# Optimization experiments

Measured on AMD Instinct MI355X. Metric: run time of the kernel, lower is better.

Reference implementation:

```python
import jax, jax.numpy as jnp
import numpy as np

B, Q, CACHE, CROSS = 16, 16, 1024, 1024
D, H, DK, DFF = 1024, 16, 64, 4096
EPS = 1e-5


def _ln(x, g, b):
    mu = jnp.mean(x, axis=-1, keepdims=True)
    var = jnp.mean(jnp.square(x - mu), axis=-1, keepdims=True)
    return (x - mu) * jax.lax.rsqrt(var + EPS) * g + b


def _heads(t):  # [B, L, D] -> [B, H, L, DK]
    return t.reshape(t.shape[0], t.shape[1], H, DK).transpose(0, 2, 1, 3)


def _attn(q, k, v, mask):  # q:[B,H,Q,DK] k,v:[B,H,L,DK] mask:[B,Q,L] bool
    scores = jnp.einsum('bhqd,bhkd->bhqk', q, k) / np.sqrt(DK).astype(np.float32)
    scores = jnp.where(mask[:, None, :, :], scores, jnp.finfo(scores.dtype).min)
    p = jax.nn.softmax(scores, axis=-1)
    o = jnp.einsum('bhqk,bhkd->bhqd', p, v)
    return o.transpose(0, 2, 1, 3).reshape(q.shape[0], q.shape[2], D)


def setup_inputs() -> dict:
    key = jax.random.key(0)
    ks = jax.random.split(key, 24)
    s = 0.02
    inp = {
        'x': jax.random.normal(ks[0], (B, Q, D), jnp.float32),
        'self_k_cache': jax.random.normal(ks[1], (B, CACHE, D), jnp.float32),
        'self_v_cache': jax.random.normal(ks[2], (B, CACHE, D), jnp.float32),
        'cross_k': jax.random.normal(ks[3], (B, CROSS, D), jnp.float32),
        'cross_v': jax.random.normal(ks[4], (B, CROSS, D), jnp.float32),
        'self_attn_mask': jnp.ones((B, Q, CACHE), jnp.bool_),
        'cross_attn_mask': jnp.ones((B, Q, CROSS), jnp.bool_),
        'ln1_g': jnp.ones((D,), jnp.float32), 'ln1_b': jnp.zeros((D,), jnp.float32),
        'ln2_g': jnp.ones((D,), jnp.float32), 'ln2_b': jnp.zeros((D,), jnp.float32),
        'ln3_g': jnp.ones((D,), jnp.float32), 'ln3_b': jnp.zeros((D,), jnp.float32),
        'wq_s': jax.random.normal(ks[5], (D, D), jnp.float32) * s, 'bq_s': jnp.zeros((D,), jnp.float32),
        'wk_s': jax.random.normal(ks[6], (D, D), jnp.float32) * s, 'bk_s': jnp.zeros((D,), jnp.float32),
        'wv_s': jax.random.normal(ks[7], (D, D), jnp.float32) * s, 'bv_s': jnp.zeros((D,), jnp.float32),
        'wo_s': jax.random.normal(ks[8], (D, D), jnp.float32) * s, 'bo_s': jnp.zeros((D,), jnp.float32),
        'wq_c': jax.random.normal(ks[9], (D, D), jnp.float32) * s, 'bq_c': jnp.zeros((D,), jnp.float32),
        'wo_c': jax.random.normal(ks[10], (D, D), jnp.float32) * s, 'bo_c': jnp.zeros((D,), jnp.float32),
        'w1': jax.random.normal(ks[11], (D, DFF), jnp.float32) * s, 'b1': jnp.zeros((DFF,), jnp.float32),
        'w2': jax.random.normal(ks[12], (DFF, D), jnp.float32) * s, 'b2': jnp.zeros((D,), jnp.float32),
    }
    return inp


def reference(x, self_k_cache, self_v_cache, cross_k, cross_v,
              self_attn_mask, cross_attn_mask,
              ln1_g, ln1_b, ln2_g, ln2_b, ln3_g, ln3_b,
              wq_s, bq_s, wk_s, bk_s, wv_s, bv_s, wo_s, bo_s,
              wq_c, bq_c, wo_c, bo_c, w1, b1, w2, b2):
    # --- self-attention with KV-cache append ---
    xn = _ln(x, ln1_g, ln1_b)
    q = xn @ wq_s + bq_s
    k_new = xn @ wk_s + bk_s
    v_new = xn @ wv_s + bv_s
    k_cache = self_k_cache.at[:, CACHE - Q:, :].set(k_new)
    v_cache = self_v_cache.at[:, CACHE - Q:, :].set(v_new)
    sa = _attn(_heads(q), _heads(k_cache), _heads(v_cache), self_attn_mask)
    x = x + (sa @ wo_s + bo_s)
    # --- cross-attention (k, v pre-projected) ---
    xn = _ln(x, ln2_g, ln2_b)
    qc = xn @ wq_c + bq_c
    ca = _attn(_heads(qc), _heads(cross_k), _heads(cross_v), cross_attn_mask)
    x = x + (ca @ wo_c + bo_c)
    # --- MLP ---
    xn = _ln(x, ln3_g, ln3_b)
    x = x + (jax.nn.gelu(xn @ w1 + b1) @ w2 + b2)
    return (x, k_cache, v_cache)
```

## Files before the change

kernel.cpp:

```cpp
#include <hip/hip_runtime.h>
#include <math.h>

#define D 1024
#define QLEN 16
#define DKH 64
#define ASPLIT 4
#define LC 256

typedef unsigned int uint;
typedef unsigned short ushort;
typedef __attribute__((ext_vector_type(8))) short bf16x8;
typedef __attribute__((ext_vector_type(4))) float f32x4;

struct GemmPtrs {
  const void* W[3];
  const float* bias[3];
  const float* res[3];
  float* C[3];
};

struct WcvtDesc { const float* src; ushort* dst; int K; int N; };
struct WcvtArgs { WcvtDesc d[8]; };

__device__ __forceinline__ ushort f2bf(float f) {
  uint u = __float_as_uint(f);
  u += 0x7fffu + ((u >> 16) & 1u);
  return (ushort)(u >> 16);
}

__device__ __forceinline__ float gelu_tanh(float x) {
  float t = 0.7978845608028654f * (x + 0.044715f * x * x * x);
  float e = __expf(2.0f * t);
  float th = 1.0f - 2.0f / (e + 1.0f);
  return 0.5f * x * (1.0f + th);
}

__global__ __launch_bounds__(256)
void wcvt_k(WcvtArgs a) {
  WcvtDesc de = a.d[blockIdx.y];
  int ntn = de.N >> 6;
  int ntiles = (de.K >> 6) * ntn;
  int tile = blockIdx.x;
  if (tile >= ntiles) return;
  int kt = tile / ntn, nt = tile - kt * ntn;
  __shared__ ushort Ls[64][72];
  int t = threadIdx.x;
  int colf4 = t & 15, rbase = t >> 4;
  #pragma unroll
  for (int u = 0; u < 4; ++u) {
    int kl = u * 16 + rbase;
    float4 w4 = *(const float4*)(de.src + (size_t)(kt*64 + kl) * de.N + nt*64 + colf4*4);
    Ls[colf4*4 + 0][kl] = f2bf(w4.x);
    Ls[colf4*4 + 1][kl] = f2bf(w4.y);
    Ls[colf4*4 + 2][kl] = f2bf(w4.z);
    Ls[colf4*4 + 3][kl] = f2bf(w4.w);
  }
  __syncthreads();
  int nl = t >> 2, c = t & 3;
  uint4 v0 = *(const uint4*)(&Ls[nl][c*16]);
  uint4 v1 = *(const uint4*)(&Ls[nl][c*16 + 8]);
  ushort* dst = de.dst + (size_t)(nt*64 + nl) * de.K + kt*64 + c*16;
  *(uint4*)(dst)     = v0;
  *(uint4*)(dst + 8) = v1;
}

__global__ __launch_bounds__(256)
void ln_k(const float* __restrict__ X, const float* __restrict__ g,
          const float* __restrict__ be, uint* __restrict__ Yb) {
  int row = blockIdx.x;
  int t = threadIdx.x;
  const float4* xp = (const float4*)(X + (size_t)row * D);
  float4 x4 = xp[t];
  float s  = x4.x + x4.y + x4.z + x4.w;
  float ss = x4.x*x4.x + x4.y*x4.y + x4.z*x4.z + x4.w*x4.w;
  #pragma unroll
  for (int off = 32; off >= 1; off >>= 1) {
    s  += __shfl_xor(s, off);
    ss += __shfl_xor(ss, off);
  }
  __shared__ float as_[4], ass_[4];
  if ((t & 63) == 0) { as_[t >> 6] = s; ass_[t >> 6] = ss; }
  __syncthreads();
  s  = as_[0] + as_[1] + as_[2] + as_[3];
  ss = ass_[0] + ass_[1] + ass_[2] + ass_[3];
  float mu   = s * (1.0f / D);
  float var  = ss * (1.0f / D) - mu * mu;
  float rstd = rsqrtf(var + 1e-5f);
  float4 g4 = ((const float4*)g)[t];
  float4 b4 = ((const float4*)be)[t];
  float y0 = (x4.x - mu) * rstd * g4.x + b4.x;
  float y1 = (x4.y - mu) * rstd * g4.y + b4.y;
  float y2 = (x4.z - mu) * rstd * g4.z + b4.z;
  float y3 = (x4.w - mu) * rstd * g4.w + b4.w;
  uint2 o;
  o.x = (uint)f2bf(y0) | ((uint)f2bf(y1) << 16);
  o.y = (uint)f2bf(y2) | ((uint)f2bf(y3) << 16);
  *(uint2*)(Yb + (size_t)row * 512 + t * 2) = o;
}

template<int ASRC>
__global__ __launch_bounds__(256)
void gemm_mfma(const void* __restrict__ Ain, GemmPtrs p, int N, int K, int S) {
  int z = blockIdx.z;
  int mat = z / S, split = z - mat * S;
  const ushort* __restrict__ WT = (const ushort*)p.W[mat];
  float* __restrict__ C = p.C[mat];
  int Ks = K / S, kb = split * Ks;
  int m0 = blockIdx.x * 64, n0 = blockIdx.y * 64;
  __shared__ short As[64 * 40];
  __shared__ short Ws[64 * 40];
  int t = threadIdx.x;
  int lane = t & 63, w = t >> 6;
  int wr = w >> 1, wc = w & 1;
  int fr = lane & 15, fg = lane >> 4;
  f32x4 acc[2][2] = {};
  int srow = t >> 2, sch = (t & 3) * 8;
  int soff = srow * 40 + sch;
  const ushort* wsrc  = WT + (size_t)(n0 + srow) * K + kb + sch;
  const ushort* asrcb = (const ushort*)Ain + (size_t)(m0 + srow) * K + kb + sch;
  const float*  asrcf = (const float*)Ain + (size_t)(m0 + srow) * K + kb + sch;

  for (int kt = 0; kt < Ks; kt += 32) {
    if (ASRC == 1) {
      *(uint4*)(As + soff) = *(const uint4*)(asrcb + kt);
    } else {
      const float* ap = asrcf + kt;
      float4 a0 = *(const float4*)ap, a1 = *(const float4*)(ap + 4);
      float av[8] = {a0.x, a0.y, a0.z, a0.w, a1.x, a1.y, a1.z, a1.w};
      uint pk[4];
      #pragma unroll
      for (int e = 0; e < 4; ++e) {
        float lo = gelu_tanh(av[2*e]), hi = gelu_tanh(av[2*e + 1]);
        pk[e] = (uint)f2bf(lo) | ((uint)f2bf(hi) << 16);
      }
      uint4 o; o.x = pk[0]; o.y = pk[1]; o.z = pk[2]; o.w = pk[3];
      *(uint4*)(As + soff) = o;
    }
    *(uint4*)(Ws + soff) = *(const uint4*)(wsrc + kt);
    __syncthreads();
    bf16x8 af[2], bfr[2];
    #pragma unroll
    for (int i = 0; i < 2; ++i)
      af[i] = *(const bf16x8*)(As + (wr*32 + i*16 + fr) * 40 + fg * 8);
    #pragma unroll
    for (int j = 0; j < 2; ++j)
      bfr[j] = *(const bf16x8*)(Ws + (wc*32 + j*16 + fr) * 40 + fg * 8);
    #pragma unroll
    for (int i = 0; i < 2; ++i)
      #pragma unroll
      for (int j = 0; j < 2; ++j)
        acc[i][j] = __builtin_amdgcn_mfma_f32_16x16x32_bf16(af[i], bfr[j], acc[i][j], 0, 0, 0);
    __syncthreads();
  }
  const float* bias = p.bias[mat];
  const float* res  = p.res[mat];
  #pragma unroll
  for (int i = 0; i < 2; ++i) {
    #pragma unroll
    for (int j = 0; j < 2; ++j) {
      int n = n0 + wc*32 + j*16 + fr;
      int mb = m0 + wr*32 + i*16 + fg*4;
      #pragma unroll
      for (int r = 0; r < 4; ++r) {
        float v = acc[i][j][r];
        if (split == 0) {
          v += bias[n];
          if (res) v += res[(size_t)(mb + r) * N + n];
        }
        atomicAdd(C + (size_t)(mb + r) * N + n, v);
      }
    }
  }
}

template<int COPY>
__global__ __launch_bounds__(256)
void attn_part(const float* __restrict__ Qm, const float* __restrict__ Km,
               const float* __restrict__ Vm,
               const float* __restrict__ Kn, const float* __restrict__ Vn,
               float* __restrict__ OutK, float* __restrict__ OutV,
               float* __restrict__ Opart, float* __restrict__ ML, int L) {
  __shared__ float Ssc[16][260];
  int bh = blockIdx.x, split = blockIdx.y;
  int b = bh >> 4, h = bh & 15;
  int tid = threadIdx.x;
  const float* qbase = Qm + (size_t)b * QLEN * D + h * DKH;
  int nb = L - QLEN;

  if (COPY) {
    #pragma unroll
    for (int u = 0; u < 16; ++u) {
      int idx = u * 256 + tid;
      int r = idx >> 4, c = idx & 15;
      int row = split * LC + r;
      size_t dsto = ((size_t)b * L + row) * 256 + h * 16 + c;
      float4 kv, vv;
      if (row < nb) {
        kv = ((const float4*)Km)[dsto];
        vv = ((const float4*)Vm)[dsto];
      } else {
        size_t so = ((size_t)b * QLEN + (row - nb)) * 256 + h * 16 + c;
        kv = ((const float4*)Kn)[so];
        vv = ((const float4*)Vn)[so];
      }
      ((float4*)OutK)[dsto] = kv;
      ((float4*)OutV)[dsto] = vv;
    }
  }

  {
    int j = split * LC + tid;
    const float* ksrc;
    if (COPY && j >= nb)
      ksrc = Kn + ((size_t)b * QLEN + (j - nb)) * D + h * DKH;
    else
      ksrc = Km + ((size_t)b * L + j) * D + h * DKH;
    const float4* kp = (const float4*)ksrc;
    float4 kr[16];
    #pragma unroll
    for (int c = 0; c < 16; ++c) kr[c] = kp[c];
    for (int qi = 0; qi < 16; ++qi) {
      const float4* qv = (const float4*)(qbase + qi * D);
      float d0 = 0.f;
      #pragma unroll
      for (int c = 0; c < 16; ++c) {
        float4 q4 = qv[c];
        d0 += q4.x*kr[c].x + q4.y*kr[c].y + q4.z*kr[c].z + q4.w*kr[c].w;
      }
      Ssc[qi][tid] = d0 * 0.125f;
    }
  }
  __syncthreads();

  {
    int row = tid >> 4, lane = tid & 15;
    float m = -1e30f;
    #pragma unroll
    for (int c = 0; c < 16; ++c) m = fmaxf(m, Ssc[row][lane + c * 16]);
    #pragma unroll
    for (int off = 8; off >= 1; off >>= 1) m = fmaxf(m, __shfl_xor(m, off));
    float l = 0.f;
    #pragma unroll
    for (int c = 0; c < 16; ++c) {
      float pv = __expf(Ssc[row][lane + c * 16] - m);
      Ssc[row][lane + c * 16] = pv;
      l += pv;
    }
    #pragma unroll
    for (int off = 8; off >= 1; off >>= 1) l += __shfl_xor(l, off);
    if (lane == 0) {
      ML[(size_t)(bh * ASPLIT + split) * 32 + row]      = m;
      ML[(size_t)(bh * ASPLIT + split) * 32 + 16 + row] = l;
    }
  }
  __syncthreads();

  {
    int d = tid & 63, qg = tid >> 6;
    float a0 = 0, a1 = 0, a2 = 0, a3 = 0;
    int lim = COPY ? (nb - split * LC) : LC;
    if (lim > LC) lim = LC;
    if (lim < 0) lim = 0;
    const float* vp = Vm + ((size_t)b * L + split * LC) * D + h * DKH + d;
    for (int j = 0; j < lim; ++j) {
      float v = vp[(size_t)j * D];
      a0 = fmaf(Ssc[qg*4+0][j], v, a0);
      a1 = fmaf(Ssc[qg*4+1][j], v, a1);
      a2 = fmaf(Ssc[qg*4+2][j], v, a2);
      a3 = fmaf(Ssc[qg*4+3][j], v, a3);
    }
    if (COPY) {
      for (int j = lim; j < LC; ++j) {
        int row = split * LC + j;
        float v = Vn[((size_t)b * QLEN + (row - nb)) * D + h * DKH + d];
        a0 = fmaf(Ssc[qg*4+0][j], v, a0);
        a1 = fmaf(Ssc[qg*4+1][j], v, a1);
        a2 = fmaf(Ssc[qg*4+2][j], v, a2);
        a3 = fmaf(Ssc[qg*4+3][j], v, a3);
      }
    }
    float* op = Opart + (size_t)(bh * ASPLIT + split) * QLEN * DKH;
    op[(qg*4+0)*DKH + d] = a0;
    op[(qg*4+1)*DKH + d] = a1;
    op[(qg*4+2)*DKH + d] = a2;
    op[(qg*4+3)*DKH + d] = a3;
  }
}

__global__ __launch_bounds__(256)
void attn_comb(const float* __restrict__ Opart, const float* __restrict__ ML,
               ushort* __restrict__ Om) {
  __shared__ float Ms[ASPLIT][16], Ls[ASPLIT][16];
  int bh = blockIdx.x;
  int b = bh >> 4, h = bh & 15;
  int tid = threadIdx.x;
  if (tid < ASPLIT * 32) {
    int s = tid >> 5, r = tid & 31;
    float v = ML[(size_t)(bh * ASPLIT + s) * 32 + r];
    if (r < 16) Ms[s][r] = v; else Ls[s][r - 16] = v;
  }
  __syncthreads();
  #pragma unroll
  for (int k = 0; k < 4; ++k) {
    int idx = k * 256 + tid;
    int qi = idx >> 6, d = idx & 63;
    float M = Ms[0][qi];
    #pragma unroll
    for (int s = 1; s < ASPLIT; ++s) M = fmaxf(M, Ms[s][qi]);
    float Lsum = 0.f, o = 0.f;
    #pragma unroll
    for (int s = 0; s < ASPLIT; ++s) {
      float w = __expf(Ms[s][qi] - M);
      Lsum += Ls[s][qi] * w;
      o += w * Opart[((size_t)(bh * ASPLIT + s) * QLEN + qi) * DKH + d];
    }
    Om[(size_t)(b * QLEN + qi) * D + h * DKH + d] = f2bf(o / Lsum);
  }
}

extern "C" void kernel_launch(void* const* d_in, const int* in_sizes, int n_in,
                              void* d_out, int out_size, void* d_ws, size_t ws_size,
                              hipStream_t stream) {
  (void)in_sizes; (void)n_in; (void)out_size; (void)ws_size;
  const float* x      = (const float*)d_in[0];
  const float* kcache = (const float*)d_in[1];
  const float* vcache = (const float*)d_in[2];
  const float* crossk = (const float*)d_in[3];
  const float* crossv = (const float*)d_in[4];
  const float* ln1g = (const float*)d_in[7];
  const float* ln1b = (const float*)d_in[8];
  const float* ln2g = (const float*)d_in[9];
  const float* ln2b = (const float*)d_in[10];
  const float* ln3g = (const float*)d_in[11];
  const float* ln3b = (const float*)d_in[12];
  const float* wq_s = (const float*)d_in[13];
  const float* bq_s = (const float*)d_in[14];
  const float* wk_s = (const float*)d_in[15];
  const float* bk_s = (const float*)d_in[16];
  const float* wv_s = (const float*)d_in[17];
  const float* bv_s = (const float*)d_in[18];
  const float* wo_s = (const float*)d_in[19];
  const float* bo_s = (const float*)d_in[20];
  const float* wq_c = (const float*)d_in[21];
  const float* bq_c = (const float*)d_in[22];
  const float* wo_c = (const float*)d_in[23];
  const float* bo_c = (const float*)d_in[24];
  const float* w1   = (const float*)d_in[25];
  const float* b1   = (const float*)d_in[26];
  const float* w2   = (const float*)d_in[27];
  const float* b2   = (const float*)d_in[28];

  float* outx = (float*)d_out;
  float* outk = outx + 262144;
  float* outv = outk + 16777216;

  float* ws = (float*)d_ws;
  float* q     = ws;
  float* kn    = ws + 1 * 262144;
  float* vn    = ws + 2 * 262144;
  float* qc    = ws + 3 * 262144;
  float* xr    = ws + 4 * 262144;
  float* hb    = ws + 5 * 262144;
  uint*  xnb   = (uint*)(ws + 2359296);
  ushort* sab  = (ushort*)(ws + 2490368);
  float* opart = ws + 2555904;
  float* ml    = ws + 3604480;
  ushort* wtb  = (ushort*)(ws + 3637248);
  ushort* wqT  = wtb;
  ushort* wkT  = wtb + 1 * 1048576;
  ushort* wvT  = wtb + 2 * 1048576;
  ushort* woT  = wtb + 3 * 1048576;
  ushort* wqcT = wtb + 4 * 1048576;
  ushort* wocT = wtb + 5 * 1048576;
  ushort* w1T  = wtb + 6 * 1048576;
  ushort* w2T  = wtb + 10 * 1048576;

  dim3 blk(256);

  hipMemsetAsync(ws, 0, (size_t)2359296 * sizeof(float), stream);
  hipMemsetAsync(outx, 0, (size_t)262144 * sizeof(float), stream);

  {
    WcvtArgs a;
    a.d[0] = {wq_s, wqT, 1024, 1024};
    a.d[1] = {wk_s, wkT, 1024, 1024};
    a.d[2] = {wv_s, wvT, 1024, 1024};
    a.d[3] = {wo_s, woT, 1024, 1024};
    a.d[4] = {wq_c, wqcT, 1024, 1024};
    a.d[5] = {wo_c, wocT, 1024, 1024};
    a.d[6] = {w1, w1T, 1024, 4096};
    a.d[7] = {w2, w2T, 4096, 1024};
    wcvt_k<<<dim3(1024, 8), blk, 0, stream>>>(a);
  }

  ln_k<<<256, blk, 0, stream>>>(x, ln1g, ln1b, xnb);

  {
    GemmPtrs p{};
    p.W[0] = wqT; p.W[1] = wkT; p.W[2] = wvT;
    p.bias[0] = bq_s; p.bias[1] = bk_s; p.bias[2] = bv_s;
    p.C[0] = q; p.C[1] = kn; p.C[2] = vn;
    gemm_mfma<1><<<dim3(4,16,12), blk, 0, stream>>>(xnb, p, 1024, 1024, 4);
  }

  attn_part<1><<<dim3(256, ASPLIT), blk, 0, stream>>>(
      q, kcache, vcache, kn, vn, outk, outv, opart, ml, 1024);
  attn_comb<<<256, blk, 0, stream>>>(opart, ml, sab);

  {
    GemmPtrs p{}; p.W[0] = woT; p.bias[0] = bo_s; p.res[0] = x; p.C[0] = xr;
    gemm_mfma<1><<<dim3(4,16,8), blk, 0, stream>>>(sab, p, 1024, 1024, 8);
  }

  ln_k<<<256, blk, 0, stream>>>(xr, ln2g, ln2b, xnb);

  {
    GemmPtrs p{}; p.W[0] = wqcT; p.bias[0] = bq_c; p.C[0] = qc;
    gemm_mfma<1><<<dim3(4,16,8), blk, 0, stream>>>(xnb, p, 1024, 1024, 8);
  }

  attn_part<0><<<dim3(256, ASPLIT), blk, 0, stream>>>(
      qc, crossk, crossv, nullptr, nullptr, nullptr, nullptr, opart, ml, 1024);
  attn_comb<<<256, blk, 0, stream>>>(opart, ml, sab);

  {
    GemmPtrs p{}; p.W[0] = wocT; p.bias[0] = bo_c; p.C[0] = xr;
    gemm_mfma<1><<<dim3(4,16,8), blk, 0, stream>>>(sab, p, 1024, 1024, 8);
  }

  ln_k<<<256, blk, 0, stream>>>(xr, ln3g, ln3b, xnb);

  {
    GemmPtrs p{}; p.W[0] = w1T; p.bias[0] = b1; p.C[0] = hb;
    gemm_mfma<1><<<dim3(4,64,2), blk, 0, stream>>>(xnb, p, 4096, 1024, 2);
  }

  {
    GemmPtrs p{}; p.W[0] = w2T; p.bias[0] = b2; p.res[0] = xr; p.C[0] = outx;
    gemm_mfma<2><<<dim3(4,16,8), blk, 0, stream>>>(hb, p, 1024, 4096, 8);
  }
}
```

Measured before the change: 649.1 us.

## Replace atomic split-K with partial buffers and fused reduce/LN/GELU kernels

Split-K GEMMs now write partial sums to per-split buffers instead of using atomicAdd. Separate reduction kernels add them up and fuse bias, residual, the following LayerNorm and GELU, which removes the memsets and the per-element GELU in the down-projection's A-load. The KV-cache append now runs as a standalone copy kernel, so attention reads the output cache directly. Attention splits go from 4 to 8 with half-width dot products. The cost is extra kernel launches and extra partial-buffer traffic.

```diff
diff --git a/kernel.cpp b/kernel.cpp
--- a/kernel.cpp
+++ b/kernel.cpp
@@ -4,8 +4,8 @@
 #define D 1024
 #define QLEN 16
 #define DKH 64
-#define ASPLIT 4
-#define LC 256
+#define ASPLIT 8
+#define LC 128
 
 typedef unsigned int uint;
 typedef unsigned short ushort;
@@ -14,13 +14,13 @@
 
 struct GemmPtrs {
   const void* W[3];
-  const float* bias[3];
-  const float* res[3];
   float* C[3];
 };
 
 struct WcvtDesc { const float* src; ushort* dst; int K; int N; };
 struct WcvtArgs { WcvtDesc d[8]; };
+
+struct Red3 { const float* P[3]; const float* bias[3]; float* out[3]; int S; };
 
 __device__ __forceinline__ ushort f2bf(float f) {
   uint u = __float_as_uint(f);
@@ -69,8 +69,7 @@
           const float* __restrict__ be, uint* __restrict__ Yb) {
   int row = blockIdx.x;
   int t = threadIdx.x;
-  const float4* xp = (const float4*)(X + (size_t)row * D);
-  float4 x4 = xp[t];
+  float4 x4 = ((const float4*)(X + (size_t)row * D))[t];
   float s  = x4.x + x4.y + x4.z + x4.w;
   float ss = x4.x*x4.x + x4.y*x4.y + x4.z*x4.z + x4.w*x4.w;
   #pragma unroll
@@ -98,13 +97,11 @@
   *(uint2*)(Yb + (size_t)row * 512 + t * 2) = o;
 }
 
-template<int ASRC>
-__global__ __launch_bounds__(256)
-void gemm_mfma(const void* __restrict__ Ain, GemmPtrs p, int N, int K, int S) {
+__global__ __launch_bounds__(256)
+void gemm_mfma(const ushort* __restrict__ A, GemmPtrs p, int N, int K, int S) {
   int z = blockIdx.z;
   int mat = z / S, split = z - mat * S;
   const ushort* __restrict__ WT = (const ushort*)p.W[mat];
-  float* __restrict__ C = p.C[mat];
   int Ks = K / S, kb = split * Ks;
   int m0 = blockIdx.x * 64, n0 = blockIdx.y * 64;
   __shared__ short As[64 * 40];
@@ -116,26 +113,11 @@
   f32x4 acc[2][2] = {};
   int srow = t >> 2, sch = (t & 3) * 8;
   int soff = srow * 40 + sch;
-  const ushort* wsrc  = WT + (size_t)(n0 + srow) * K + kb + sch;
-  const ushort* asrcb = (const ushort*)Ain + (size_t)(m0 + srow) * K + kb + sch;
-  const float*  asrcf = (const float*)Ain + (size_t)(m0 + srow) * K + kb + sch;
+  const ushort* wsrc = WT + (size_t)(n0 + srow) * K + kb + sch;
+  const ushort* asrc = A + (size_t)(m0 + srow) * K + kb + sch;
 
   for (int kt = 0; kt < Ks; kt += 32) {
-    if (ASRC == 1) {
-      *(uint4*)(As + soff) = *(const uint4*)(asrcb + kt);
-    } else {
-      const float* ap = asrcf + kt;
-      float4 a0 = *(const float4*)ap, a1 = *(const float4*)(ap + 4);
-      float av[8] = {a0.x, a0.y, a0.z, a0.w, a1.x, a1.y, a1.z, a1.w};
-      uint pk[4];
-      #pragma unroll
-      for (int e = 0; e < 4; ++e) {
-        float lo = gelu_tanh(av[2*e]), hi = gelu_tanh(av[2*e + 1]);
-        pk[e] = (uint)f2bf(lo) | ((uint)f2bf(hi) << 16);
-      }
-      uint4 o; o.x = pk[0]; o.y = pk[1]; o.z = pk[2]; o.w = pk[3];
-      *(uint4*)(As + soff) = o;
-    }
+    *(uint4*)(As + soff) = *(const uint4*)(asrc + kt);
     *(uint4*)(Ws + soff) = *(const uint4*)(wsrc + kt);
     __syncthreads();
     bf16x8 af[2], bfr[2];
@@ -152,8 +134,7 @@
         acc[i][j] = __builtin_amdgcn_mfma_f32_16x16x32_bf16(af[i], bfr[j], acc[i][j], 0, 0, 0);
     __syncthreads();
   }
-  const float* bias = p.bias[mat];
-  const float* res  = p.res[mat];
+  float* P = p.C[mat] + (size_t)split * 256 * N;
   #pragma unroll
   for (int i = 0; i < 2; ++i) {
     #pragma unroll
@@ -161,73 +142,148 @@
       int n = n0 + wc*32 + j*16 + fr;
       int mb = m0 + wr*32 + i*16 + fg*4;
       #pragma unroll
-      for (int r = 0; r < 4; ++r) {
-        float v = acc[i][j][r];
-        if (split == 0) {
-          v += bias[n];
-          if (res) v += res[(size_t)(mb + r) * N + n];
-        }
-        atomicAdd(C + (size_t)(mb + r) * N + n, v);
-      }
-    }
-  }
-}
-
-template<int COPY>
+      for (int r = 0; r < 4; ++r)
+        P[(size_t)(mb + r) * N + n] = acc[i][j][r];
+    }
+  }
+}
+
+__global__ __launch_bounds__(256)
+void red3_k(Red3 a) {
+  int mat = blockIdx.y, row = blockIdx.x, t = threadIdx.x;
+  const float* P = a.P[mat];
+  float4 v = ((const float4*)a.bias[mat])[t];
+  for (int s = 0; s < a.S; ++s) {
+    float4 u = ((const float4*)(P + ((size_t)s * 256 + row) * 1024))[t];
+    v.x += u.x; v.y += u.y; v.z += u.z; v.w += u.w;
+  }
+  ((float4*)(a.out[mat] + (size_t)row * 1024))[t] = v;
+}
+
+__global__ __launch_bounds__(256)
+void redln_k(const float* __restrict__ P, int S, const float* __restrict__ bias,
+             const float* __restrict__ res, float* __restrict__ Xout,
+             uint* __restrict__ Yb, const float* __restrict__ g,
+             const float* __restrict__ be) {
+  int row = blockIdx.x, t = threadIdx.x;
+  float4 v = ((const float4*)bias)[t];
+  float4 rr = ((const float4*)(res + (size_t)row * 1024))[t];
+  v.x += rr.x; v.y += rr.y; v.z += rr.z; v.w += rr.w;
+  for (int s = 0; s < S; ++s) {
+    float4 u = ((const float4*)(P + ((size_t)s * 256 + row) * 1024))[t];
+    v.x += u.x; v.y += u.y; v.z += u.z; v.w += u.w;
+  }
+  ((float4*)(Xout + (size_t)row * 1024))[t] = v;
+  float s1 = v.x + v.y + v.z + v.w;
+  float ss = v.x*v.x + v.y*v.y + v.z*v.z + v.w*v.w;
+  #pragma unroll
+  for (int off = 32; off >= 1; off >>= 1) {
+    s1 += __shfl_xor(s1, off);
+    ss += __shfl_xor(ss, off);
+  }
+  __shared__ float as_[4], ass_[4];
+  if ((t & 63) == 0) { as_[t >> 6] = s1; ass_[t >> 6] = ss; }
+  __syncthreads();
+  s1 = as_[0] + as_[1] + as_[2] + as_[3];
+  ss = ass_[0] + ass_[1] + ass_[2] + ass_[3];
+  float mu   = s1 * (1.0f / D);
+  float var  = ss * (1.0f / D) - mu * mu;
+  float rstd = rsqrtf(var + 1e-5f);
+  float4 g4 = ((const float4*)g)[t];
+  float4 b4 = ((const float4*)be)[t];
+  float y0 = (v.x - mu) * rstd * g4.x + b4.x;
+  float y1 = (v.y - mu) * rstd * g4.y + b4.y;
+  float y2 = (v.z - mu) * rstd * g4.z + b4.z;
+  float y3 = (v.w - mu) * rstd * g4.w + b4.w;
+  uint2 o;
+  o.x = (uint)f2bf(y0) | ((uint)f2bf(y1) << 16);
+  o.y = (uint)f2bf(y2) | ((uint)f2bf(y3) << 16);
+  *(uint2*)(Yb + (size_t)row * 512 + t * 2) = o;
+}
+
+__global__ __launch_bounds__(256)
+void redgelu_k(const float* __restrict__ P, int S, const float* __restrict__ bias,
+               uint* __restrict__ Hb) {
+  int row = blockIdx.x, t = threadIdx.x;
+  #pragma unroll
+  for (int u = 0; u < 4; ++u) {
+    int idx = u * 256 + t;
+    float4 v = ((const float4*)bias)[idx];
+    for (int s = 0; s < S; ++s) {
+      float4 q = ((const float4*)(P + ((size_t)s * 256 + row) * 4096))[idx];
+      v.x += q.x; v.y += q.y; v.z += q.z; v.w += q.w;
+    }
+    v.x = gelu_tanh(v.x); v.y = gelu_tanh(v.y);
+    v.z = gelu_tanh(v.z); v.w = gelu_tanh(v.w);
+    uint2 o;
+    o.x = (uint)f2bf(v.x) | ((uint)f2bf(v.y) << 16);
+    o.y = (uint)f2bf(v.z) | ((uint)f2bf(v.w) << 16);
+    *(uint2*)(Hb + (size_t)row * 2048 + idx * 2) = o;
+  }
+}
+
+__global__ __launch_bounds__(256)
+void redfin_k(const float* __restrict__ P, int S, const float* __restrict__ bias,
+              const float* __restrict__ res, float* __restrict__ out) {
+  int row = blockIdx.x, t = threadIdx.x;
+  float4 v = ((const float4*)bias)[t];
+  float4 rr = ((const float4*)(res + (size_t)row * 1024))[t];
+  v.x += rr.x; v.y += rr.y; v.z += rr.z; v.w += rr.w;
+  for (int s = 0; s < S; ++s) {
+    float4 u = ((const float4*)(P + ((size_t)s * 256 + row) * 1024))[t];
+    v.x += u.x; v.y += u.y; v.z += u.z; v.w += u.w;
+  }
+  ((float4*)(out + (size_t)row * 1024))[t] = v;
+}
+
+__global__ __launch_bounds__(256)
+void cache_build2(const float4* __restrict__ kin, const float4* __restrict__ knew,
+                  float4* __restrict__ kout,
+                  const float4* __restrict__ vin, const float4* __restrict__ vnew,
+                  float4* __restrict__ vout) {
+  size_t i = (size_t)blockIdx.x * 256 + threadIdx.x;
+  const float4* cin; const float4* nv; float4* co;
+  if (i < 4194304) { cin = kin; nv = knew; co = kout; }
+  else { i -= 4194304; cin = vin; nv = vnew; co = vout; }
+  size_t row = (i >> 8) & 1023;
+  float4 v;
+  if (row < 1008) {
+    v = cin[i];
+  } else {
+    size_t b   = i >> 18;
+    size_t col = i & 255;
+    v = nv[(b * QLEN + (row - 1008)) * 256 + col];
+  }
+  co[i] = v;
+}
+
 __global__ __launch_bounds__(256)
 void attn_part(const float* __restrict__ Qm, const float* __restrict__ Km,
-               const float* __restrict__ Vm,
-               const float* __restrict__ Kn, const float* __restrict__ Vn,
-               float* __restrict__ OutK, float* __restrict__ OutV,
-               float* __restrict__ Opart, float* __restrict__ ML, int L) {
-  __shared__ float Ssc[16][260];
+               const float* __restrict__ Vm, float* __restrict__ Opart,
+               float* __restrict__ ML, int L) {
+  __shared__ float Ssc[16][136];
   int bh = blockIdx.x, split = blockIdx.y;
   int b = bh >> 4, h = bh & 15;
   int tid = threadIdx.x;
   const float* qbase = Qm + (size_t)b * QLEN * D + h * DKH;
-  int nb = L - QLEN;
-
-  if (COPY) {
-    #pragma unroll
-    for (int u = 0; u < 16; ++u) {
-      int idx = u * 256 + tid;
-      int r = idx >> 4, c = idx & 15;
-      int row = split * LC + r;
-      size_t dsto = ((size_t)b * L + row) * 256 + h * 16 + c;
-      float4 kv, vv;
-      if (row < nb) {
-        kv = ((const float4*)Km)[dsto];
-        vv = ((const float4*)Vm)[dsto];
-      } else {
-        size_t so = ((size_t)b * QLEN + (row - nb)) * 256 + h * 16 + c;
-        kv = ((const float4*)Kn)[so];
-        vv = ((const float4*)Vn)[so];
-      }
-      ((float4*)OutK)[dsto] = kv;
-      ((float4*)OutV)[dsto] = vv;
-    }
-  }
-
-  {
-    int j = split * LC + tid;
-    const float* ksrc;
-    if (COPY && j >= nb)
-      ksrc = Kn + ((size_t)b * QLEN + (j - nb)) * D + h * DKH;
-    else
-      ksrc = Km + ((size_t)b * L + j) * D + h * DKH;
-    const float4* kp = (const float4*)ksrc;
-    float4 kr[16];
-    #pragma unroll
-    for (int c = 0; c < 16; ++c) kr[c] = kp[c];
+
+  {
+    int j = tid >> 1, half = tid & 1;
+    int row = split * LC + j;
+    const float4* kp = (const float4*)(Km + ((size_t)b * L + row) * D + h * DKH + half * 32);
+    float4 kr[8];
+    #pragma unroll
+    for (int c = 0; c < 8; ++c) kr[c] = kp[c];
     for (int qi = 0; qi < 16; ++qi) {
-      const float4* qv = (const float4*)(qbase + qi * D);
+      const float4* qv = (const float4*)(qbase + qi * D + half * 32);
       float d0 = 0.f;
       #pragma unroll
-      for (int c = 0; c < 16; ++c) {
+      for (int c = 0; c < 8; ++c) {
         float4 q4 = qv[c];
         d0 += q4.x*kr[c].x + q4.y*kr[c].y + q4.z*kr[c].z + q4.w*kr[c].w;
       }
-      Ssc[qi][tid] = d0 * 0.125f;
+      d0 += __shfl_xor(d0, 1);
+      if (!half) Ssc[qi][j] = d0 * 0.125f;
     }
   }
   __syncthreads();
@@ -236,12 +292,12 @@
     int row = tid >> 4, lane = tid & 15;
     float m = -1e30f;
     #pragma unroll
-    for (int c = 0; c < 16; ++c) m = fmaxf(m, Ssc[row][lane + c * 16]);
+    for (int c = 0; c < 8; ++c) m = fmaxf(m, Ssc[row][lane + c * 16]);
     #pragma unroll
     for (int off = 8; off >= 1; off >>= 1) m = fmaxf(m, __shfl_xor(m, off));
     float l = 0.f;
     #pragma unroll
-    for (int c = 0; c < 16; ++c) {
+    for (int c = 0; c < 8; ++c) {
       float pv = __expf(Ssc[row][lane + c * 16] - m);
       Ssc[row][lane + c * 16] = pv;
       l += pv;
@@ -258,26 +314,13 @@
   {
     int d = tid & 63, qg = tid >> 6;
     float a0 = 0, a1 = 0, a2 = 0, a3 = 0;
-    int lim = COPY ? (nb - split * LC) : LC;
-    if (lim > LC) lim = LC;
-    if (lim < 0) lim = 0;
     const float* vp = Vm + ((size_t)b * L + split * LC) * D + h * DKH + d;
-    for (int j = 0; j < lim; ++j) {
+    for (int j = 0; j < LC; ++j) {
       float v = vp[(size_t)j * D];
       a0 = fmaf(Ssc[qg*4+0][j], v, a0);
       a1 = fmaf(Ssc[qg*4+1][j], v, a1);
       a2 = fmaf(Ssc[qg*4+2][j], v, a2);
       a3 = fmaf(Ssc[qg*4+3][j], v, a3);
-    }
-    if (COPY) {
-      for (int j = lim; j < LC; ++j) {
-        int row = split * LC + j;
-        float v = Vn[((size_t)b * QLEN + (row - nb)) * D + h * DKH + d];
-        a0 = fmaf(Ssc[qg*4+0][j], v, a0);
-        a1 = fmaf(Ssc[qg*4+1][j], v, a1);
-        a2 = fmaf(Ssc[qg*4+2][j], v, a2);
-        a3 = fmaf(Ssc[qg*4+3][j], v, a3);
-      }
     }
     float* op = Opart + (size_t)(bh * ASPLIT + split) * QLEN * DKH;
     op[(qg*4+0)*DKH + d] = a0;
@@ -294,7 +337,7 @@
   int bh = blockIdx.x;
   int b = bh >> 4, h = bh & 15;
   int tid = threadIdx.x;
-  if (tid < ASPLIT * 32) {
+  {
     int s = tid >> 5, r = tid & 31;
     float v = ML[(size_t)(bh * ASPLIT + s) * 32 + r];
     if (r < 16) Ms[s][r] = v; else Ls[s][r - 16] = v;
@@ -355,17 +398,24 @@
   float* outv = outk + 16777216;
 
   float* ws = (float*)d_ws;
-  float* q     = ws;
-  float* kn    = ws + 1 * 262144;
-  float* vn    = ws + 2 * 262144;
-  float* qc    = ws + 3 * 262144;
-  float* xr    = ws + 4 * 262144;
-  float* hb    = ws + 5 * 262144;
-  uint*  xnb   = (uint*)(ws + 2359296);
-  ushort* sab  = (ushort*)(ws + 2490368);
-  float* opart = ws + 2555904;
-  float* ml    = ws + 3604480;
-  ushort* wtb  = (ushort*)(ws + 3637248);
+  float* qP    = ws;
+  float* knP   = ws + 1048576;
+  float* vnP   = ws + 2097152;
+  float* q     = ws + 3145728;
+  float* kn    = ws + 3407872;
+  float* vn    = ws + 3670016;
+  float* qc    = ws + 3932160;
+  float* xr    = ws + 4194304;
+  float* xr2   = ws + 4456448;
+  uint*  xnb   = (uint*)(ws + 4718592);
+  ushort* sab  = (ushort*)(ws + 4849664);
+  uint*  hbb   = (uint*)(ws + 4915200);
+  float* opart = ws + 5439488;
+  float* ml    = ws + 7536640;
+  float* oP    = ws + 7602176;
+  float* qcP   = ws + 9699328;
+  float* upP   = ws + 11796480;
+  ushort* wtb  = (ushort*)(ws + 13893632);
   ushort* wqT  = wtb;
   ushort* wkT  = wtb + 1 * 1048576;
   ushort* wvT  = wtb + 2 * 1048576;
@@ -376,9 +426,6 @@
   ushort* w2T  = wtb + 10 * 1048576;
 
   dim3 blk(256);
-
-  hipMemsetAsync(ws, 0, (size_t)2359296 * sizeof(float), stream);
-  hipMemsetAsync(outx, 0, (size_t)262144 * sizeof(float), stream);
 
   {
     WcvtArgs a;
@@ -398,45 +445,59 @@
   {
     GemmPtrs p{};
     p.W[0] = wqT; p.W[1] = wkT; p.W[2] = wvT;
-    p.bias[0] = bq_s; p.bias[1] = bk_s; p.bias[2] = bv_s;
-    p.C[0] = q; p.C[1] = kn; p.C[2] = vn;
-    gemm_mfma<1><<<dim3(4,16,12), blk, 0, stream>>>(xnb, p, 1024, 1024, 4);
-  }
-
-  attn_part<1><<<dim3(256, ASPLIT), blk, 0, stream>>>(
-      q, kcache, vcache, kn, vn, outk, outv, opart, ml, 1024);
+    p.C[0] = qP; p.C[1] = knP; p.C[2] = vnP;
+    gemm_mfma<<<dim3(4,16,12), blk, 0, stream>>>((const ushort*)xnb, p, 1024, 1024, 4);
+  }
+  {
+    Red3 a;
+    a.P[0] = qP; a.P[1] = knP; a.P[2] = vnP;
+    a.bias[0] = bq_s; a.bias[1] = bk_s; a.bias[2] = bv_s;
+    a.out[0] = q; a.out[1] = kn; a.out[2] = vn;
+    a.S = 4;
+    red3_k<<<dim3(256, 3), blk, 0, stream>>>(a);
+  }
+
+  cache_build2<<<32768, blk, 0, stream>>>(
+      (const float4*)kcache, (const float4*)kn, (float4*)outk,
+      (const float4*)vcache, (const float4*)vn, (float4*)outv);
+
+  attn_part<<<dim3(256, ASPLIT), blk, 0, stream>>>(q, outk, outv, opart, ml, 1024);
   attn_comb<<<256, blk, 0, stream>>>(opart, ml, sab);
 
   {
-    GemmPtrs p{}; p.W[0] = woT; p.bias[0] = bo_s; p.res[0] = x; p.C[0] = xr;
-    gemm_mfma<1><<<dim3(4,16,8), blk, 0, stream>>>(sab, p, 1024, 1024, 8);
-  }
-
-  ln_k<<<256, blk, 0, stream>>>(xr, ln2g, ln2b, xnb);
-
-  {
-    GemmPtrs p{}; p.W[0] = wqcT; p.bias[0] = bq_c; p.C[0] = qc;
-    gemm_mfma<1><<<dim3(4,16,8), blk, 0, stream>>>(xnb, p, 1024, 1024, 8);
-  }
-
-  attn_part<0><<<dim3(256, ASPLIT), blk, 0, stream>>>(
-      qc, crossk, crossv, nullptr, nullptr, nullptr, nullptr, opart, ml, 1024);
+    GemmPtrs p{}; p.W[0] = woT; p.C[0] = oP;
+    gemm_mfma<<<dim3(4,16,8), blk, 0, stream>>>(sab, p, 1024, 1024, 8);
+  }
+  redln_k<<<256, blk, 0, stream>>>(oP, 8, bo_s, x, xr, xnb, ln2g, ln2b);
+
+  {
+    GemmPtrs p{}; p.W[0] = wqcT; p.C[0] = qcP;
+    gemm_mfma<<<dim3(4,16,8), blk, 0, stream>>>((const ushort*)xnb, p, 1024, 1024, 8);
+  }
+  {
+    Red3 a;
+    a.P[0] = qcP; a.bias[0] = bq_c; a.out[0] = qc; a.S = 8;
+    red3_k<<<dim3(256, 1), blk, 0, stream>>>(a);
+  }
+
+  attn_part<<<dim3(256, ASPLIT), blk, 0, stream>>>(qc, crossk, crossv, opart, ml, 1024);
   attn_comb<<<256, blk, 0, stream>>>(opart, ml, sab);
 
   {
-    GemmPtrs p{}; p.W[0] = wocT; p.bias[0] = bo_c; p.C[0] = xr;
-    gemm_mfma<1><<<dim3(4,16,8), blk, 0, stream>>>(sab, p, 1024, 1024, 8);
-  }
-
-  ln_k<<<256, blk, 0, stream>>>(xr, ln3g, ln3b, xnb);
-
-  {
-    GemmPtrs p{}; p.W[0] = w1T; p.bias[0] = b1; p.C[0] = hb;
-    gemm_mfma<1><<<dim3(4,64,2), blk, 0, stream>>>(xnb, p, 4096, 1024, 2);
-  }
-
-  {
-    GemmPtrs p{}; p.W[0] = w2T; p.bias[0] = b2; p.res[0] = xr; p.C[0] = outx;
-    gemm_mfma<2><<<dim3(4,16,8), blk, 0, stream>>>(hb, p, 1024, 4096, 8);
-  }
-}
+    GemmPtrs p{}; p.W[0] = wocT; p.C[0] = oP;
+    gemm_mfma<<<dim3(4,16,8), blk, 0, stream>>>(sab, p, 1024, 1024, 8);
+  }
+  redln_k<<<256, blk, 0, stream>>>(oP, 8, bo_c, xr, xr2, xnb, ln3g, ln3b);
+
+  {
+    GemmPtrs p{}; p.W[0] = w1T; p.C[0] = upP;
+    gemm_mfma<<<dim3(4,64,2), blk, 0, stream>>>((const ushort*)xnb, p, 4096, 1024, 2);
+  }
+  redgelu_k<<<256, blk, 0, stream>>>(upP, 2, b1, hbb);
+
+  {
+    GemmPtrs p{}; p.W[0] = w2T; p.C[0] = oP;
+    gemm_mfma<<<dim3(4,16,8), blk, 0, stream>>>((const ushort*)hbb, p, 1024, 4096, 8);
+  }
+  redfin_k<<<256, blk, 0, stream>>>(oP, 8, b2, xr2, outx);
+}
```

Result: faster. 632.8 us (-2.5%).
